# Optimization experiments

Measured on AMD Instinct MI355X. Metric: run time of the kernel, lower is better.

The kernel has to match this reference:

```python
import jax, jax.numpy as jnp
import numpy as np

EPS = 1e-5
H, W, D_FULL, D_RFFT, DIM = 9, 11, 9, 5, 900  # spectral grid 9x11x9, rfft last dim -> 5

def layer_norm(x, gamma, beta):
    mu = jnp.mean(x, axis=-1, keepdims=True)
    var = jnp.var(x, axis=-1, keepdims=True)
    return (x - mu) * jax.lax.rsqrt(var + EPS) * gamma + beta

def setup_inputs() -> dict:
    key = jax.random.key(0)
    ks = jax.random.split(key, 12)
    B, N, C = 64, H * W * D_FULL, DIM  # N = 891
    hidden, rank = int(C * 2.0), C // 2  # 1800, 450
    return {
        "x": jax.random.normal(ks[0], (B, N, C), dtype=jnp.float32),
        # Global_Filter complex weight: (h, w, d, dim, 2), init ~ N(0,1)*0.02
        "cw": jax.random.normal(ks[1], (H, W, D_RFFT, C, 2), dtype=jnp.float32) * 0.02,
        "gamma1": jnp.ones((C,), jnp.float32),
        "beta1": jnp.zeros((C,), jnp.float32),
        "gamma2": jnp.ones((C,), jnp.float32),
        "beta2": jnp.zeros((C,), jnp.float32),
        # low-rank MLP (torch Linear weights are (out, in); we apply x @ W.T)
        "u1_w": jax.random.normal(ks[2], (rank, C), jnp.float32) * (1.0 / np.sqrt(C)),
        "v1_w": jax.random.normal(ks[3], (hidden, rank), jnp.float32) * (1.0 / np.sqrt(rank)),
        "v1_b": jnp.zeros((hidden,), jnp.float32),
        "u2_w": jax.random.normal(ks[4], (rank, hidden), jnp.float32) * (1.0 / np.sqrt(hidden)),
        "v2_w": jax.random.normal(ks[5], (C, rank), jnp.float32) * (1.0 / np.sqrt(rank)),
        "v2_b": jnp.zeros((C,), jnp.float32),
    }

def reference(x, cw, gamma1, beta1, gamma2, beta2, u1_w, v1_w, v1_b, u2_w, v2_w, v2_b):
    B, N, C = x.shape
    # norm1 -> global spectral filter
    y = layer_norm(x, gamma1, beta1)
    y = y.reshape(B, H, W, D_FULL, C)
    yf = jnp.fft.rfftn(y, axes=(1, 2, 3), norm="ortho")  # (B, 9, 11, 5, C) complex
    weight = jax.lax.complex(cw[..., 0], cw[..., 1])      # (9, 11, 5, C)
    yf = yf * weight
    y = jnp.fft.irfftn(yf, s=(H, W, D_FULL), axes=(1, 2, 3), norm="ortho")
    y = y.reshape(B, N, C)
    # norm2 -> low-rank MLP (dropout/droppath = identity in eval)
    z = layer_norm(y, gamma2, beta2)
    z = jnp.einsum("bnc,rc->bnr", z, u1_w)
    z = jnp.einsum("bnr,hr->bnh", z, v1_w) + v1_b
    z = jax.nn.gelu(z, approximate=False)
    z = jnp.einsum("bnh,rh->bnr", z, u2_w)
    z = jnp.einsum("bnr,cr->bnc", z, v2_w) + v2_b
    return x + z
```

## Files before the change

### kernel.cpp

```cpp
#include <hip/hip_runtime.h>


typedef unsigned short u16;
typedef __bf16 bf16x8 __attribute__((ext_vector_type(8)));
typedef float f32x4 __attribute__((ext_vector_type(4)));

#define LN_EPS 1e-5f
#define CH 16

constexpr float KC9[9] = {
  1.0f, 0.766044443118978f, 0.17364817766693041f, -0.4999999999999998f,
  -0.9396926207859083f, -0.9396926207859084f, -0.5000000000000004f,
  0.17364817766692997f, 0.7660444431189778f };
constexpr float KS9[9] = {
  0.0f, 0.6427876096865393f, 0.984807753012208f, 0.8660254037844387f,
  0.3420201433256689f, -0.34202014332566866f, -0.8660254037844385f,
  -0.9848077530122081f, -0.6427876096865396f };
constexpr float KC11[11] = {
  1.0f, 0.8412535328311812f, 0.41541501300188644f, -0.14231483827328512f,
  -0.654860733945285f, -0.9594929736144974f, -0.9594929736144974f,
  -0.6548607339452852f, -0.14231483827328543f, 0.4154150130018863f,
  0.8412535328311811f };
constexpr float KS11[11] = {
  0.0f, 0.5406408174555976f, 0.9096319953545183f, 0.9898214418809327f,
  0.7557495743542583f, 0.2817325568414297f, -0.2817325568414296f,
  -0.7557495743542582f, -0.9898214418809327f, -0.9096319953545184f,
  -0.5406408174555979f };

__device__ __forceinline__ u16 f2bf(float f) {
  unsigned int u = __float_as_uint(f);
  return (u16)((u + 0x7fffu + ((u >> 16) & 1u)) >> 16);
}
__device__ __forceinline__ float gelu_f(float v) {
  float t = 0.7978845608028654f * v * (1.f + 0.044715f * v * v);
  float e = __expf(2.f * t);
  float th = 1.f - 2.f * __builtin_amdgcn_rcpf(e + 1.f);
  return 0.5f * v * (1.f + th);
}

__global__ __launch_bounds__(256) void k_cvt(const float* __restrict__ s, u16* __restrict__ d,
                                             int rows, int sc, int dc,
                                             const float* __restrict__ gamma) {
  int i = blockIdx.x * 256 + threadIdx.x;
  if (i >= rows * dc) return;
  int r = i / dc, c = i % dc;
  u16 o = 0;
  if (c < sc) {
    float v = s[(size_t)r * sc + c];
    if (gamma) v *= gamma[c];
    o = f2bf(v);
  }
  d[i] = o;
}

__global__ __launch_bounds__(256) void k_bias1(const float* __restrict__ u1w,
                                               const float* __restrict__ b2,
                                               float* __restrict__ out) {
  int r = blockIdx.x * 256 + threadIdx.x;
  if (r < 450) {
    float s = 0.f;
    for (int c = 0; c < 900; c++) s += u1w[r * 900 + c] * b2[c];
    out[r] = s;
  }
}

__global__ __launch_bounds__(256) void k_stats1(const float* __restrict__ x,
                                                float2* __restrict__ stats) {
  int tok = blockIdx.x * 4 + (threadIdx.x >> 6);
  int l = threadIdx.x & 63;
  const float* row = x + (size_t)tok * 900;
  float s1 = 0.f, s2 = 0.f;
#pragma unroll
  for (int j = 0; j < 15; j++) {
    int c = l + j * 64;
    if (c < 900) { float a = row[c]; s1 += a; s2 += a * a; }
  }
#pragma unroll
  for (int off = 32; off; off >>= 1) { s1 += __shfl_xor(s1, off, 64); s2 += __shfl_xor(s2, off, 64); }
  if (l == 0) {
    float m = s1 * (1.f / 900.f);
    float var = s2 * (1.f / 900.f) - m * m;
    stats[tok] = make_float2(m, rsqrtf(var + LN_EPS));
  }
}

__global__ __launch_bounds__(256) void k_spectral(const float* __restrict__ x,
                                                  const float2* __restrict__ stats,
                                                  const float* __restrict__ g1,
                                                  const float* __restrict__ b1,
                                                  const float* __restrict__ cw,
                                                  float* __restrict__ y) {
  __shared__ float sre[5 * 99 * CH];
  __shared__ float sim[5 * 99 * CH];
  int b = blockIdx.x / 57, cc = blockIdx.x % 57;
  int c0 = cc * CH;
  int t = threadIdx.x;
  const float* xb = x + (size_t)b * 801900;
  const float2* st = stats + (size_t)b * 891;

  for (int col = t; col < 99 * CH; col += 256) {
    int pos = col / CH, c = col % CH;
    int cg = c0 + c; bool ok = cg < 900;
    float g = ok ? g1[cg] : 0.f, be = ok ? b1[cg] : 0.f;
    float yv[9];
#pragma unroll
    for (int d = 0; d < 9; d++) {
      float a = ok ? xb[(size_t)(pos * 9 + d) * 900 + cg] : 0.f;
      float2 s = st[pos * 9 + d];
      yv[d] = (a - s.x) * s.y * g + be;
    }
#pragma unroll
    for (int kd = 0; kd < 5; kd++) {
      float re = 0.f, im = 0.f;
#pragma unroll
      for (int d = 0; d < 9; d++) { int j = (kd * d) % 9; re += yv[d] * KC9[j]; im -= yv[d] * KS9[j]; }
      sre[(kd * 99 + pos) * CH + c] = re;
      sim[(kd * 99 + pos) * CH + c] = im;
    }
  }
  __syncthreads();

  for (int col = t; col < 5 * 9 * CH; col += 256) {
    int kd = col / (9 * CH), r = col % (9 * CH), h = r / CH, c = r % CH;
    int base = (kd * 99 + h * 11) * CH + c;
    float xr[11], xi[11];
#pragma unroll
    for (int w = 0; w < 11; w++) { xr[w] = sre[base + w * CH]; xi[w] = sim[base + w * CH]; }
#pragma unroll
    for (int k = 0; k < 11; k++) {
      float yr = 0.f, yi = 0.f;
#pragma unroll
      for (int w = 0; w < 11; w++) {
        int j = (k * w) % 11; float cf = KC11[j], sf = KS11[j];
        yr += xr[w] * cf + xi[w] * sf;
        yi += xi[w] * cf - xr[w] * sf;
      }
      sre[base + k * CH] = yr; sim[base + k * CH] = yi;
    }
  }
  __syncthreads();

  for (int col = t; col < 5 * 11 * CH; col += 256) {
    int kd = col / (11 * CH), r = col % (11 * CH), kw = r / CH, c = r % CH;
    int cg = c0 + c;
    int base = (kd * 99 + kw) * CH + c;
    float xr[9], xi[9];
#pragma unroll
    for (int h = 0; h < 9; h++) { xr[h] = sre[base + h * 11 * CH]; xi[h] = sim[base + h * 11 * CH]; }
    float zr[9], zi[9];
#pragma unroll
    for (int k = 0; k < 9; k++) {
      float yr = 0.f, yi = 0.f;
#pragma unroll
      for (int h = 0; h < 9; h++) {
        int j = (k * h) % 9; float cf = KC9[j], sf = KS9[j];
        yr += xr[h] * cf + xi[h] * sf;
        yi += xi[h] * cf - xr[h] * sf;
      }
      float wr = 0.f, wi = 0.f;
      if (cg < 900) {
        size_t widx = ((size_t)((k * 11 + kw) * 5 + kd) * 900 + cg) * 2;
        wr = cw[widx]; wi = cw[widx + 1];
      }
      zr[k] = yr * wr - yi * wi;
      zi[k] = yr * wi + yi * wr;
    }
#pragma unroll
    for (int h = 0; h < 9; h++) {
      float orr = 0.f, oi = 0.f;
#pragma unroll
      for (int k = 0; k < 9; k++) {
        int j = (k * h) % 9; float cf = KC9[j], sf = KS9[j];
        orr += zr[k] * cf - zi[k] * sf;
        oi  += zi[k] * cf + zr[k] * sf;
      }
      sre[base + h * 11 * CH] = orr; sim[base + h * 11 * CH] = oi;
    }
  }
  __syncthreads();

  for (int col = t; col < 5 * 9 * CH; col += 256) {
    int kd = col / (9 * CH), r = col % (9 * CH), h = r / CH, c = r % CH;
    int base = (kd * 99 + h * 11) * CH + c;
    float xr[11], xi[11];
#pragma unroll
    for (int w = 0; w < 11; w++) { xr[w] = sre[base + w * CH]; xi[w] = sim[base + w * CH]; }
#pragma unroll
    for (int k = 0; k < 11; k++) {
      float yr = 0.f, yi = 0.f;
#pragma unroll
      for (int w = 0; w < 11; w++) {
        int j = (k * w) % 11; float cf = KC11[j], sf = KS11[j];
        yr += xr[w] * cf - xi[w] * sf;
        yi += xi[w] * cf + xr[w] * sf;
      }
      sre[base + k * CH] = yr; sim[base + k * CH] = yi;
    }
  }
  __syncthreads();

  for (int col = t; col < 99 * CH; col += 256) {
    int pos = col / CH, c = col % CH;
    int cg = c0 + c;
    if (cg >= 900) continue;
    float Xr[5], Xi[5];
#pragma unroll
    for (int k = 0; k < 5; k++) { Xr[k] = sre[(k * 99 + pos) * CH + c]; Xi[k] = sim[(k * 99 + pos) * CH + c]; }
#pragma unroll
    for (int d = 0; d < 9; d++) {
      float acc = Xr[0];
#pragma unroll
      for (int k = 1; k < 5; k++) { int j = (k * d) % 9; acc += 2.f * (Xr[k] * KC9[j] - Xi[k] * KS9[j]); }
      y[((size_t)b * 891 + pos * 9 + d) * 900 + cg] = acc * (1.f / 891.f);
    }
  }
}

__global__ __launch_bounds__(256) void k_ln2(const float* __restrict__ y, u16* __restrict__ yn) {
  int tok = blockIdx.x * 4 + (threadIdx.x >> 6);
  int l = threadIdx.x & 63;
  const float* row = y + (size_t)tok * 900;
  float v[15];
  float s1 = 0.f, s2 = 0.f;
#pragma unroll
  for (int j = 0; j < 15; j++) {
    int c = l + j * 64;
    float a = (c < 900) ? row[c] : 0.f;
    v[j] = a; s1 += a; s2 += a * a;
  }
#pragma unroll
  for (int off = 32; off; off >>= 1) { s1 += __shfl_xor(s1, off, 64); s2 += __shfl_xor(s2, off, 64); }
  float m = s1 * (1.f / 900.f);
  float var = s2 * (1.f / 900.f) - m * m;
  float rs = rsqrtf(var + LN_EPS);
  u16* orow = yn + (size_t)tok * 928;
#pragma unroll
  for (int j = 0; j < 15; j++) {
    int c = l + j * 64;
    if (c < 900) orow[c] = f2bf((v[j] - m) * rs);
    else if (c < 928) orow[c] = 0;
  }
}

typedef __attribute__((address_space(1))) void gvoid;
typedef __attribute__((address_space(3))) void svoid;

__device__ __forceinline__ void stage16(const u16* g, u16* lbase) {
  __builtin_amdgcn_global_load_lds((gvoid*)(void*)g, (svoid*)lbase, 16, 0, 0);
}

__device__ __forceinline__ void stage_tile(const u16* __restrict__ A, const u16* __restrict__ B,
                                           int m0, int n0, int M, int N, int ldk, int k0,
                                           u16* As, u16* Bs, int w, int l) {
  int arow = (w << 4) + (l >> 2);
  int koff = k0 + (((l & 3) ^ ((l >> 3) & 3)) << 3);
#pragma unroll
  for (int j = 0; j < 2; j++) {
    int r = (j << 6) + arow;
    int gm = m0 + r; gm = gm < M ? gm : M - 1;
    stage16(A + (size_t)gm * ldk + koff, &As[((j << 6) + (w << 4)) * 32]);
    int gn = n0 + r; gn = gn < N ? gn : N - 1;
    stage16(B + (size_t)gn * ldk + koff, &Bs[((j << 6) + (w << 4)) * 32]);
  }
}

template <int EPI>
__global__ __launch_bounds__(256, 2) void k_gemm(
    const u16* __restrict__ A, const u16* __restrict__ B,
    int M, int N, int Kt, int ldk, int NT,
    u16* __restrict__ Ob, int ldo, int Nstore,
    const float* __restrict__ bias,
    const float* __restrict__ Xres, float* __restrict__ Of) {
  __shared__ u16 As[2][128 * 32];
  __shared__ u16 Bs[2][128 * 32];
  int t = threadIdx.x, w = t >> 6, l = t & 63;

  int nblk = gridDim.x;
  int xcd = blockIdx.x & 7, idx = blockIdx.x >> 3;
  int q = nblk >> 3, r8 = nblk & 7;
  int lin = (xcd < r8 ? xcd * (q + 1) : r8 * (q + 1) + (xcd - r8) * q) + idx;
  int mt = lin / NT, nt = lin % NT;

  int m0 = mt * 128, n0 = nt * 128;
  int wm = (w >> 1) << 6, wn = (w & 1) << 6;
  int fr = l & 15, fq = l >> 4;
  int rsw = ((fq ^ ((fr >> 1) & 3)) << 3);

  f32x4 acc[4][4];
  f32x4 zero = {0.f, 0.f, 0.f, 0.f};
#pragma unroll
  for (int i = 0; i < 4; i++)
#pragma unroll
    for (int j = 0; j < 4; j++) acc[i][j] = zero;

  stage_tile(A, B, m0, n0, M, N, ldk, 0, As[0], Bs[0], w, l);
  if (Kt > 1) stage_tile(A, B, m0, n0, M, N, ldk, 32, As[1], Bs[1], w, l);

  for (int kt = 0; kt < Kt; ++kt) {
    if (kt + 1 < Kt) asm volatile("s_waitcnt vmcnt(4)\n\ts_barrier" ::: "memory");
    else             asm volatile("s_waitcnt vmcnt(0)\n\ts_barrier" ::: "memory");

    const u16* as = As[kt & 1];
    const u16* bs = Bs[kt & 1];
    bf16x8 af[4], bfr[4];
#pragma unroll
    for (int i = 0; i < 4; i++) af[i] = *(const bf16x8*)&as[(wm + (i << 4) + fr) * 32 + rsw];
#pragma unroll
    for (int i = 0; i < 4; i++) bfr[i] = *(const bf16x8*)&bs[(wn + (i << 4) + fr) * 32 + rsw];
#pragma unroll
    for (int i = 0; i < 4; i++)
#pragma unroll
      for (int j = 0; j < 4; j++)
        acc[i][j] = __builtin_amdgcn_mfma_f32_16x16x32_bf16(af[i], bfr[j], acc[i][j], 0, 0, 0);

    asm volatile("s_barrier" ::: "memory");
    if (kt + 2 < Kt)
      stage_tile(A, B, m0, n0, M, N, ldk, (kt + 2) * 32, As[kt & 1], Bs[kt & 1], w, l);
  }

#pragma unroll
  for (int j = 0; j < 4; j++) {
    int gn = n0 + wn + (j << 4) + fr;
    float bv = 0.f;
    if (EPI != 2) bv = (gn < Nstore) ? bias[gn] : 0.f;
#pragma unroll
    for (int i = 0; i < 4; i++) {
#pragma unroll
      for (int r = 0; r < 4; r++) {
        int gm = m0 + wm + (i << 4) + (fq << 2) + r;
        if (gm < M) {
          float val = acc[i][j][r] + bv;
          if (EPI == 1) val = gelu_f(val);
          if (EPI == 3) {
            if (gn < Nstore) Of[(size_t)gm * Nstore + gn] = val + Xres[(size_t)gm * Nstore + gn];
          } else {
            if (gn < ldo) Ob[(size_t)gm * ldo + gn] = (gn < Nstore) ? f2bf(val) : (u16)0;
          }
        }
      }
    }
  }
}

extern "C" void kernel_launch(void* const* d_in, const int* in_sizes, int n_in,
                              void* d_out, int out_size, void* d_ws, size_t ws_size,
                              hipStream_t stream) {
  const float* x   = (const float*)d_in[0];
  const float* cw  = (const float*)d_in[1];
  const float* g1  = (const float*)d_in[2];
  const float* b1  = (const float*)d_in[3];
  const float* g2  = (const float*)d_in[4];
  const float* b2  = (const float*)d_in[5];
  const float* u1w = (const float*)d_in[6];
  const float* v1w = (const float*)d_in[7];
  const float* v1b = (const float*)d_in[8];
  const float* u2w = (const float*)d_in[9];
  const float* v2w = (const float*)d_in[10];
  const float* v2b = (const float*)d_in[11];

  char* ws = (char*)d_ws;
  float* y   = (float*)ws;
  u16*   t2  = (u16*)ws;
  u16*   t3  = (u16*)(ws + 228096000);
  u16*   u1g = (u16*)(ws + 286488576);
  u16*   v1c = (u16*)(ws + 287323776);
  u16*   u2c = (u16*)(ws + 289166976);
  u16*   v2c = (u16*)(ws + 290808576);
  float* b1r = (float*)(ws + 291730176);

  u16*    yn    = (u16*)d_out;
  u16*    t1    = (u16*)((char*)d_out + 105836544);
  float2* stats = (float2*)((char*)d_out + 164229120);
  float*  outF  = (float*)d_out;

  k_cvt<<<1632, 256, 0, stream>>>(u1w, u1g, 450, 900, 928, g2);
  k_cvt<<<3600, 256, 0, stream>>>(v1w, v1c, 1800, 450, 512, nullptr);
  k_cvt<<<3207, 256, 0, stream>>>(u2w, u2c, 450, 1800, 1824, nullptr);
  k_cvt<<<1800, 256, 0, stream>>>(v2w, v2c, 900, 450, 512, nullptr);
  k_bias1<<<2, 256, 0, stream>>>(u1w, b2, b1r);

  k_stats1<<<14256, 256, 0, stream>>>(x, stats);
  k_spectral<<<64 * 57, 256, 0, stream>>>(x, stats, g1, b1, cw, y);
  k_ln2<<<14256, 256, 0, stream>>>(y, yn);

  k_gemm<0><<<446 * 4,  256, 0, stream>>>(yn, u1g, 57024, 450,  29, 928,  4,  t1, 512, 450, b1r, nullptr, nullptr);
  k_gemm<1><<<446 * 15, 256, 0, stream>>>(t1, v1c, 57024, 1800, 16, 512,  15, t2, 1824, 1800, v1b, nullptr, nullptr);
  k_gemm<2><<<446 * 4,  256, 0, stream>>>(t2, u2c, 57024, 450,  57, 1824, 4,  t3, 512, 450, nullptr, nullptr, nullptr);
  k_gemm<3><<<446 * 8,  256, 0, stream>>>(t3, v2c, 57024, 900,  16, 512,  8,  nullptr, 0, 900, v2b, x, outF);
}
```

Measured before the change: 1.456 ms.

## Widen GEMM tiles to 128x512 with 1024-thread blocks and triple-buffered LDS

The bf16 MFMA GEMM moves from 128x128 tiles on 256-thread blocks to 128x512 tiles on 1024-thread blocks. Each of the 16 waves still computes a 64x64 sub-tile, so each A tile is loaded once per block and reused across four times as many output columns, cutting redundant A traffic. The LDS pipeline goes from double to triple buffering, with per-thread vmcnt waits adjusted because only half the threads stage A. MFMA issue is raised with s_setprio. In exchange, the large LDS footprint allows only one block per CU. Each block's barriers now sync 16 waves, and the N=450 GEMMs launch only 446 blocks, which risks poor CU balance and tail effects. The N=1800 GEMM also pads to 2048 columns, which wastes compute.

Result: slower. 1.542 ms (+5.9%).

```diff
diff --git a/kernel.cpp b/kernel.cpp
--- a/kernel.cpp
+++ b/kernel.cpp
@@ -249,30 +249,15 @@
   __builtin_amdgcn_global_load_lds((gvoid*)(void*)g, (svoid*)lbase, 16, 0, 0);
 }
 
-__device__ __forceinline__ void stage_tile(const u16* __restrict__ A, const u16* __restrict__ B,
-                                           int m0, int n0, int M, int N, int ldk, int k0,
-                                           u16* As, u16* Bs, int w, int l) {
-  int arow = (w << 4) + (l >> 2);
-  int koff = k0 + (((l & 3) ^ ((l >> 3) & 3)) << 3);
-#pragma unroll
-  for (int j = 0; j < 2; j++) {
-    int r = (j << 6) + arow;
-    int gm = m0 + r; gm = gm < M ? gm : M - 1;
-    stage16(A + (size_t)gm * ldk + koff, &As[((j << 6) + (w << 4)) * 32]);
-    int gn = n0 + r; gn = gn < N ? gn : N - 1;
-    stage16(B + (size_t)gn * ldk + koff, &Bs[((j << 6) + (w << 4)) * 32]);
-  }
-}
-
 template <int EPI>
-__global__ __launch_bounds__(256, 2) void k_gemm(
+__global__ __launch_bounds__(1024, 4) void k_gemm(
     const u16* __restrict__ A, const u16* __restrict__ B,
     int M, int N, int Kt, int ldk, int NT,
     u16* __restrict__ Ob, int ldo, int Nstore,
     const float* __restrict__ bias,
     const float* __restrict__ Xres, float* __restrict__ Of) {
-  __shared__ u16 As[2][128 * 32];
-  __shared__ u16 Bs[2][128 * 32];
+  __shared__ __align__(16) u16 As[3][128 * 32];
+  __shared__ __align__(16) u16 Bs[3][512 * 32];
   int t = threadIdx.x, w = t >> 6, l = t & 63;
 
   int nblk = gridDim.x;
@@ -281,11 +266,29 @@
   int lin = (xcd < r8 ? xcd * (q + 1) : r8 * (q + 1) + (xcd - r8) * q) + idx;
   int mt = lin / NT, nt = lin % NT;
 
-  int m0 = mt * 128, n0 = nt * 128;
-  int wm = (w >> 1) << 6, wn = (w & 1) << 6;
+  int m0 = mt << 7, n0 = nt << 9;
+  int wm = (w >> 3) << 6;
+  int wn = (w & 7) << 6;
   int fr = l & 15, fq = l >> 4;
   int rsw = ((fq ^ ((fr >> 1) & 3)) << 3);
 
+  bool lead = (t < 512);
+  int koffs = (((t & 3) ^ ((t >> 3) & 3)) << 3);
+  int ar = t >> 2;
+  int br0 = t >> 2, br1 = br0 + 256;
+
+  auto stage = [&](int kt, int buf) {
+    int k0 = kt << 5;
+    int gn0 = n0 + br0; gn0 = gn0 < N ? gn0 : N - 1;
+    stage16(B + (size_t)gn0 * ldk + k0 + koffs, &Bs[buf][t << 3]);
+    int gn1 = n0 + br1; gn1 = gn1 < N ? gn1 : N - 1;
+    stage16(B + (size_t)gn1 * ldk + k0 + koffs, &Bs[buf][(t + 1024) << 3]);
+    if (lead) {
+      int gm = m0 + ar; gm = gm < M ? gm : M - 1;
+      stage16(A + (size_t)gm * ldk + k0 + koffs, &As[buf][t << 3]);
+    }
+  };
+
   f32x4 acc[4][4];
   f32x4 zero = {0.f, 0.f, 0.f, 0.f};
 #pragma unroll
@@ -293,29 +296,39 @@
 #pragma unroll
     for (int j = 0; j < 4; j++) acc[i][j] = zero;
 
-  stage_tile(A, B, m0, n0, M, N, ldk, 0, As[0], Bs[0], w, l);
-  if (Kt > 1) stage_tile(A, B, m0, n0, M, N, ldk, 32, As[1], Bs[1], w, l);
+  stage(0, 0);
+  if (Kt > 1) stage(1, 1);
+  if (Kt > 2) stage(2, 2);
 
   for (int kt = 0; kt < Kt; ++kt) {
-    if (kt + 1 < Kt) asm volatile("s_waitcnt vmcnt(4)\n\ts_barrier" ::: "memory");
-    else             asm volatile("s_waitcnt vmcnt(0)\n\ts_barrier" ::: "memory");
-
-    const u16* as = As[kt & 1];
-    const u16* bs = Bs[kt & 1];
-    bf16x8 af[4], bfr[4];
+    if (kt + 2 < Kt) {
+      if (lead) asm volatile("s_waitcnt vmcnt(6)\n\ts_barrier" ::: "memory");
+      else      asm volatile("s_waitcnt vmcnt(4)\n\ts_barrier" ::: "memory");
+    } else if (kt + 1 < Kt) {
+      if (lead) asm volatile("s_waitcnt vmcnt(3)\n\ts_barrier" ::: "memory");
+      else      asm volatile("s_waitcnt vmcnt(2)\n\ts_barrier" ::: "memory");
+    } else {
+      asm volatile("s_waitcnt vmcnt(0)\n\ts_barrier" ::: "memory");
+    }
+
+    int buf = kt % 3;
+    const u16* as = As[buf];
+    const u16* bs = Bs[buf];
+    bf16x8 af[4], bfv[4];
 #pragma unroll
     for (int i = 0; i < 4; i++) af[i] = *(const bf16x8*)&as[(wm + (i << 4) + fr) * 32 + rsw];
 #pragma unroll
-    for (int i = 0; i < 4; i++) bfr[i] = *(const bf16x8*)&bs[(wn + (i << 4) + fr) * 32 + rsw];
+    for (int j = 0; j < 4; j++) bfv[j] = *(const bf16x8*)&bs[(wn + (j << 4) + fr) * 32 + rsw];
+    __builtin_amdgcn_s_setprio(1);
 #pragma unroll
     for (int i = 0; i < 4; i++)
 #pragma unroll
       for (int j = 0; j < 4; j++)
-        acc[i][j] = __builtin_amdgcn_mfma_f32_16x16x32_bf16(af[i], bfr[j], acc[i][j], 0, 0, 0);
+        acc[i][j] = __builtin_amdgcn_mfma_f32_16x16x32_bf16(af[i], bfv[j], acc[i][j], 0, 0, 0);
+    __builtin_amdgcn_s_setprio(0);
 
     asm volatile("s_barrier" ::: "memory");
-    if (kt + 2 < Kt)
-      stage_tile(A, B, m0, n0, M, N, ldk, (kt + 2) * 32, As[kt & 1], Bs[kt & 1], w, l);
+    if (kt + 3 < Kt) stage(kt + 3, buf);
   }
 
 #pragma unroll
@@ -383,8 +396,8 @@
   k_spectral<<<64 * 57, 256, 0, stream>>>(x, stats, g1, b1, cw, y);
   k_ln2<<<14256, 256, 0, stream>>>(y, yn);
 
-  k_gemm<0><<<446 * 4,  256, 0, stream>>>(yn, u1g, 57024, 450,  29, 928,  4,  t1, 512, 450, b1r, nullptr, nullptr);
-  k_gemm<1><<<446 * 15, 256, 0, stream>>>(t1, v1c, 57024, 1800, 16, 512,  15, t2, 1824, 1800, v1b, nullptr, nullptr);
-  k_gemm<2><<<446 * 4,  256, 0, stream>>>(t2, u2c, 57024, 450,  57, 1824, 4,  t3, 512, 450, nullptr, nullptr, nullptr);
-  k_gemm<3><<<446 * 8,  256, 0, stream>>>(t3, v2c, 57024, 900,  16, 512,  8,  nullptr, 0, 900, v2b, x, outF);
-}
+  k_gemm<0><<<446 * 1, 1024, 0, stream>>>(yn, u1g, 57024, 450,  29, 928,  1, t1, 512, 450, b1r, nullptr, nullptr);
+  k_gemm<1><<<446 * 4, 1024, 0, stream>>>(t1, v1c, 57024, 1800, 16, 512,  4, t2, 1824, 1800, v1b, nullptr, nullptr);
+  k_gemm<2><<<446 * 1, 1024, 0, stream>>>(t2, u2c, 57024, 450,  57, 1824, 1, t3, 512, 450, nullptr, nullptr, nullptr);
+  k_gemm<3><<<446 * 2, 1024, 0, stream>>>(t3, v2c, 57024, 900,  16, 512,  2, nullptr, 0, 900, v2b, x, outF);
+}
```
